# Kernel tuning notes

Hardware: AMD Instinct MI355X
Metric: run time of the kernel (lower is better)

Reference implementation:

```python
import jax, jax.numpy as jnp
import numpy as np

N_HEADS = 8


def setup_inputs() -> dict:
    key = jax.random.key(0)
    ks = jax.random.split(key, 6)
    B, U, Lx, Ly = 16, 512, 1024, 1024
    x = jax.random.normal(ks[0], (B, U, Lx), dtype=jnp.float32)
    y = jax.random.normal(ks[1], (B, U, Ly), dtype=jnp.float32)
    xy_mask = jax.random.randint(ks[2], (B, Lx, Ly), 0, 2).astype(jnp.bool_)
    wq = jax.random.normal(ks[3], (U, U), dtype=jnp.float32) * (1.0 / np.sqrt(U))
    wk = jax.random.normal(ks[4], (U, U), dtype=jnp.float32) * (1.0 / np.sqrt(U))
    wo = jax.random.normal(ks[5], (U, U), dtype=jnp.float32) * (1.0 / np.sqrt(U))
    return {"x": x, "y": y, "xy_mask": xy_mask, "wq": wq, "wk": wk, "wo": wo}


def reference(x, y, xy_mask, wq, wk, wo):
    # x: (B, U, Lx), y: (B, U, Ly), xy_mask: (B, Lx, Ly)
    B, U, Lx = x.shape
    Ly = y.shape[2]
    H = N_HEADS
    d = U // H
    scale = 1.0 / (d ** 0.5)

    # 1x1 conv (bias=False) == channel-mixing matmul; weight layout (out, in)
    Q = jnp.einsum('ou,bul->bol', wq, x)   # (B, U, Lx)
    K = jnp.einsum('ou,bul->bol', wk, y)   # (B, U, Ly)

    # split channels into heads (head-major channel order, matching torch.split)
    Qh = Q.reshape(B, H, d, Lx)
    Kh = K.reshape(B, H, d, Ly)

    # ReLU-scored attention with mask (no softmax)
    A = jnp.einsum('bhdx,bhdy->bhxy', Qh, Kh)           # (B, H, Lx, Ly)
    A = jnp.maximum(A, 0.0) * scale
    A = jnp.where(xy_mask[:, None, :, :], A, 0.0)

    C = jnp.einsum('bhxy,bhdy->bhdx', A, Kh).reshape(B, U, Lx)

    # per-row element-count normalization (rows with zero count use 1)
    n_el = jnp.maximum(jnp.sum(xy_mask, axis=2), 1)     # (B, Lx)
    C = C / n_el[:, None, :].astype(x.dtype)

    E = 0.5 * (Q + C)
    return jnp.einsum('ou,bul->bol', wo, E)
```

## Files before the change

### kernel.cpp

```cpp
#include <hip/hip_runtime.h>
#include <stdint.h>
#include <stddef.h>

#define B_  16
#define U_  512
#define LX_ 1024
#define LY_ 1024
#define H_  8
#define D_  64

typedef unsigned short ushort_t;
typedef unsigned int   uint_t;
typedef __bf16 v8bf  __attribute__((ext_vector_type(8)));
typedef float  v16f  __attribute__((ext_vector_type(16)));

__device__ __forceinline__ ushort_t bf16u(float f) {
    uint_t u = __float_as_uint(f);
    uint_t r = (u + 0x7FFFu + ((u >> 16) & 1u)) >> 16;
    return (ushort_t)r;
}
__device__ __forceinline__ float bfu2f(ushort_t u) {
    return __uint_as_float(((uint_t)u) << 16);
}
__device__ __forceinline__ uint_t pkbf16(float f0, float f1) {
    uint_t u0 = __float_as_uint(f0), u1 = __float_as_uint(f1);
    u0 = u0 + 0x7FFFu + ((u0 >> 16) & 1u);
    u1 = u1 + 0x7FFFu + ((u1 >> 16) & 1u);
    return __builtin_amdgcn_perm(u1, u0, 0x07060302u);
}
__device__ __forceinline__ void gload16(const void* g, void* l) {
    auto gp = (const __attribute__((address_space(1))) uint32_t*)(uintptr_t)g;
    auto lp = (__attribute__((address_space(3))) uint32_t*)(uintptr_t)l;
    __builtin_amdgcn_global_load_lds(gp, lp, 16, 0, 0);
}

__global__ void detect_kernel(const uint_t* __restrict__ mask, int* __restrict__ flag) {
    __shared__ int s;
    if (threadIdx.x == 0) s = 0;
    __syncthreads();
    int c = 0;
    for (int i = threadIdx.x; i < 1024; i += 256) c += (mask[i] <= 1u) ? 1 : 0;
    atomicAdd(&s, c);
    __syncthreads();
    if (threadIdx.x == 0) *flag = (s >= 1000) ? 1 : 0;
}

__global__ __launch_bounds__(256) void nelmask_kernel(const void* __restrict__ mask,
                                                      const int* __restrict__ flag,
                                                      float* __restrict__ nel,
                                                      uint_t* __restrict__ mb) {
    int row  = blockIdx.x * 4 + (threadIdx.x >> 6);
    int lane = threadIdx.x & 63;
    const int isInt = *flag;
    const uint8_t* m8  = (const uint8_t*)mask + (size_t)row * LY_;
    const int*     m32 = (const int*)mask + (size_t)row * LY_;
    int cnt = 0;
    for (int yg = 0; yg < LY_ / 64; ++yg) {
        int y = yg * 64 + lane;
        bool p = isInt ? (m32[y] != 0) : (m8[y] != 0);
        unsigned long long bal = __ballot(p);
        if (lane == 0) {
            mb[(size_t)row * 32 + yg * 2]     = (uint_t)bal;
            mb[(size_t)row * 32 + yg * 2 + 1] = (uint_t)(bal >> 32);
            cnt += __popcll(bal);
        }
    }
    if (lane == 0) nel[row] = (float)(cnt > 0 ? cnt : 1);
}

__global__ __launch_bounds__(256) void castw_kernel(const float* __restrict__ w0,
                                                    const float* __restrict__ w1,
                                                    const float* __restrict__ w2,
                                                    ushort_t* __restrict__ o0,
                                                    ushort_t* __restrict__ o1,
                                                    ushort_t* __restrict__ o2) {
    const float* s = blockIdx.y == 0 ? w0 : (blockIdx.y == 1 ? w1 : w2);
    ushort_t*    d = blockIdx.y == 0 ? o0 : (blockIdx.y == 1 ? o1 : o2);
    int i = (blockIdx.x * 256 + threadIdx.x) * 4;
    float4 v = *(const float4*)&s[i];
    ushort4 p;
    p.x = bf16u(v.x); p.y = bf16u(v.y); p.z = bf16u(v.z); p.w = bf16u(v.w);
    *(ushort4*)&d[i] = p;
}

__global__ __launch_bounds__(256) void castT_kernel(const float* __restrict__ X,
                                                    const float* __restrict__ Y,
                                                    ushort_t* __restrict__ XT,
                                                    ushort_t* __restrict__ YT) {
    const int l0 = blockIdx.x * 64;
    const int u0 = blockIdx.y * 64;
    const int b  = blockIdx.z & 15;
    const int sel = blockIdx.z >> 4;
    const float* S = sel ? Y : X;
    ushort_t*  Dst = sel ? YT : XT;
    __shared__ ushort_t T[64][72];
    const int tid = threadIdx.x;
    #pragma unroll
    for (int e = 0; e < 4; ++e) {
        int ci = e * 256 + tid;
        int r = ci >> 4, c4 = (ci & 15) * 4;
        float4 v = *(const float4*)&S[((size_t)(b * U_ + u0 + r) << 10) + l0 + c4];
        T[r][c4 + 0] = bf16u(v.x); T[r][c4 + 1] = bf16u(v.y);
        T[r][c4 + 2] = bf16u(v.z); T[r][c4 + 3] = bf16u(v.w);
    }
    __syncthreads();
    #pragma unroll
    for (int e = 0; e < 2; ++e) {
        int ci = e * 256 + tid;
        int lr = ci >> 3, cc = ci & 7;
        ushort_t tmp[8];
        #pragma unroll
        for (int j = 0; j < 8; ++j) tmp[j] = T[cc * 8 + j][lr];
        *(uint4*)&Dst[((size_t)((b << 10) + l0 + lr)) * U_ + u0 + cc * 8] = *(uint4*)tmp;
    }
}

template <int OUTF32>
__global__ __launch_bounds__(256) void gemm_mfma(const ushort_t* __restrict__ A, size_t aStr,
                                                 const ushort_t* __restrict__ Bm, size_t bStr,
                                                 void* __restrict__ Out, size_t oStr, int ldOut) {
    const int n0 = blockIdx.x * 128;
    const int m0 = blockIdx.y * 128;
    const int b  = blockIdx.z;
    __shared__ __align__(16) ushort_t As[128 * 64];
    __shared__ __align__(16) ushort_t Bs[128 * 64];
    const int tid = threadIdx.x;
    const ushort_t* Ab = A + aStr * b;
    const ushort_t* Bb = Bm + bStr * b;

    const int w = tid >> 6, lane = tid & 63, lo = lane & 31, hi = lane >> 5;
    const int wm = (w >> 1) * 64, wn = (w & 1) * 64;

    v16f acc00, acc01, acc10, acc11;
    #pragma unroll
    for (int i = 0; i < 16; ++i) { acc00[i] = 0.f; acc01[i] = 0.f; acc10[i] = 0.f; acc11[i] = 0.f; }

    for (int kk = 0; kk < 8; ++kk) {
        const int k0 = kk * 64;
        #pragma unroll
        for (int e = 0; e < 4; ++e) {
            int ci = e * 256 + tid;
            int r = ci >> 3, c = ci & 7;
            int g = (c ^ (r & 7)) << 3;
            gload16(&Ab[(size_t)(m0 + r) * U_ + k0 + g], &As[ci * 8]);
            gload16(&Bb[(size_t)(n0 + r) * U_ + k0 + g], &Bs[ci * 8]);
        }
        __syncthreads();
        #pragma unroll
        for (int ks = 0; ks < 4; ++ks) {
            int ch = ks * 2 + hi;
            int rA0 = wm + lo, rA1 = wm + 32 + lo;
            int rB0 = wn + lo, rB1 = wn + 32 + lo;
            v8bf a0 = *(v8bf*)&As[rA0 * 64 + ((ch ^ (rA0 & 7)) << 3)];
            v8bf a1 = *(v8bf*)&As[rA1 * 64 + ((ch ^ (rA1 & 7)) << 3)];
            v8bf b0 = *(v8bf*)&Bs[rB0 * 64 + ((ch ^ (rB0 & 7)) << 3)];
            v8bf b1 = *(v8bf*)&Bs[rB1 * 64 + ((ch ^ (rB1 & 7)) << 3)];
            acc00 = __builtin_amdgcn_mfma_f32_32x32x16_bf16(a0, b0, acc00, 0, 0, 0);
            acc01 = __builtin_amdgcn_mfma_f32_32x32x16_bf16(a0, b1, acc01, 0, 0, 0);
            acc10 = __builtin_amdgcn_mfma_f32_32x32x16_bf16(a1, b0, acc10, 0, 0, 0);
            acc11 = __builtin_amdgcn_mfma_f32_32x32x16_bf16(a1, b1, acc11, 0, 0, 0);
        }
        __syncthreads();
    }

    #pragma unroll
    for (int mi = 0; mi < 2; ++mi) {
        #pragma unroll
        for (int nj = 0; nj < 2; ++nj) {
            v16f c = mi ? (nj ? acc11 : acc10) : (nj ? acc01 : acc00);
            int n = n0 + wn + nj * 32 + lo;
            #pragma unroll
            for (int r = 0; r < 16; ++r) {
                int m = m0 + wm + mi * 32 + (r & 3) + 8 * (r >> 2) + 4 * hi;
                size_t addr = oStr * b + (size_t)m * ldOut + n;
                if (OUTF32) ((float*)Out)[addr] = c[r];
                else        ((ushort_t*)Out)[addr] = bf16u(c[r]);
            }
        }
    }
}

__global__ __launch_bounds__(256) void ktranspose_kernel(const ushort_t* __restrict__ Ka,
                                                         ushort_t* __restrict__ Kb) {
    const int y0 = blockIdx.x * 64;
    const int h  = blockIdx.y;
    const int b  = blockIdx.z;
    __shared__ ushort_t T[64][72];
    const int tid = threadIdx.x;

    #pragma unroll
    for (int e = 0; e < 2; ++e) {
        int idx = e * 256 + tid;
        int d = idx >> 3, c = idx & 7;
        uint4 v = *(const uint4*)&Ka[((size_t)(b * U_ + h * D_ + d) << 10) + y0 + c * 8];
        *(uint4*)&T[d][c * 8] = v;
    }
    __syncthreads();
    #pragma unroll
    for (int e = 0; e < 2; ++e) {
        int idx = e * 256 + tid;
        int yy = idx >> 3, dc = idx & 7;
        ushort_t tmp[8];
        #pragma unroll
        for (int j = 0; j < 8; ++j) tmp[j] = T[dc * 8 + j][yy];
        *(uint4*)&Kb[(((size_t)(b * H_ + h) << 10) + y0 + yy) * D_ + dc * 8] = *(uint4*)tmp;
    }
}

typedef uint_t v2u __attribute__((ext_vector_type(2)));

__device__ __forceinline__ void conv_sblock(const v16f& s, uint_t wbh, v8bf* fr) {
    uint_t pk[8];
    #pragma unroll
    for (int i = 0; i < 8; ++i) {
        float f0 = fmaxf(s[2 * i + 0], 0.f);
        float f1 = fmaxf(s[2 * i + 1], 0.f);
        uint_t r;
        asm("v_cvt_pk_bf16_f32 %0, %1, %2" : "=v"(r) : "v"(f0), "v"(f1));
        pk[i] = r;
    }
    #pragma unroll
    for (int t = 0; t < 2; ++t) {
        auto ra = __builtin_amdgcn_permlane32_swap(pk[4 * t + 0], pk[4 * t + 2], false, false);
        auto rb = __builtin_amdgcn_permlane32_swap(pk[4 * t + 1], pk[4 * t + 3], false, false);
        uint_t w0 = ra[0];
        uint_t w1 = rb[0];
        uint_t w2 = ra[1];
        uint_t w3 = rb[1];
        uint_t u0 = wbh >> (t * 16 + 0);
        uint_t u1 = wbh >> (t * 16 + 2);
        uint_t u2 = wbh >> (t * 16 + 4);
        uint_t u3 = wbh >> (t * 16 + 6);
        w0 &= ((u0 & 1u) * 0xFFFFu) | ((u0 & 2u) * 0x7FFF8000u);
        w1 &= ((u1 & 1u) * 0xFFFFu) | ((u1 & 2u) * 0x7FFF8000u);
        w2 &= ((u2 & 1u) * 0xFFFFu) | ((u2 & 2u) * 0x7FFF8000u);
        w3 &= ((u3 & 1u) * 0xFFFFu) | ((u3 & 2u) * 0x7FFF8000u);
        union { uint_t u[4]; v8bf b; } cv;
        cv.u[0] = w0; cv.u[1] = w1; cv.u[2] = w2; cv.u[3] = w3;
        fr[t] = cv.b;
    }
}

__global__ __launch_bounds__(256, 2) void attn_mfma(const ushort_t* __restrict__ QTg,
                                                    const ushort_t* __restrict__ Ka_g,
                                                    const ushort_t* __restrict__ Kb_g,
                                                    const uint_t* __restrict__ mbits,
                                                    const float* __restrict__ nel,
                                                    ushort_t* __restrict__ ETg) {
    const int tid = threadIdx.x;
    const int id  = blockIdx.x;
    const int bh  = id & 127;
    const int x0g = (id >> 7) * 128;
    const int b = bh >> 3, h = bh & 7;

    __shared__ __align__(16) ushort_t SM[8192 + 2 * 4096 + 2 * 4096];
    ushort_t* Qt = SM;
    ushort_t* KB = SM + 8192;
    ushort_t* KA = SM + 16384;

    const int w    = tid >> 6;
    const int lane = tid & 63;
    const int lo   = lane & 31;
    const int hi   = lane >> 5;
    const int yw   = w & 1;
    const int xws  = (w >> 1) * 64;

    const ushort_t* Qsrc   = QTg + ((size_t)(b * LX_ + x0g)) * U_ + h * D_;
    const ushort_t* KaBase = Ka_g + ((size_t)(b * U_ + h * D_)) * LY_;
    const ushort_t* KbBase = Kb_g + ((size_t)(b * H_ + h)) * LY_ * D_;
    const int bx = b * LX_ + x0g;

    #pragma unroll
    for (int e = 0; e < 4; ++e) {
        int ci = e * 256 + tid;
        int r = ci >> 3, c = ci & 7;
        gload16(&Qsrc[(size_t)r * U_ + ((c ^ (r & 7)) << 3)], &Qt[ci * 8]);
    }
    #pragma unroll
    for (int e = 0; e < 2; ++e) {
        int ci = e * 256 + tid;
        int r = ci >> 3, c = ci & 7;
        int g8 = (c ^ (r & 7)) << 3;
        gload16(&KbBase[(size_t)r * D_ + g8], &KB[ci * 8]);
        gload16(&KaBase[(size_t)r * LY_ + g8], &KA[ci * 8]);
    }
    __syncthreads();

    v8bf qf0[4], qf1[4];
    {
        int rB0 = xws + lo, rB1 = xws + 32 + lo;
        #pragma unroll
        for (int kt = 0; kt < 4; ++kt) {
            int ch = kt * 2 + hi;
            qf0[kt] = *(v8bf*)&Qt[rB0 * 64 + ((ch ^ (rB0 & 7)) << 3)];
            qf1[kt] = *(v8bf*)&Qt[rB1 * 64 + ((ch ^ (rB1 & 7)) << 3)];
        }
    }

    v16f acc00, acc01, acc10, acc11;
    #pragma unroll
    for (int i = 0; i < 16; ++i) { acc00[i] = 0.f; acc01[i] = 0.f; acc10[i] = 0.f; acc11[i] = 0.f; }

    const int rowA = yw * 32 + lo;

    for (int tt = 0; tt < 16; ++tt) {
        const int y0 = tt * 64;
        ushort_t* KBc = KB + (tt & 1) * 4096;
        ushort_t* KAc = KA + (tt & 1) * 4096;

        if (tt < 15) {
            ushort_t* KBn = KB + ((tt + 1) & 1) * 4096;
            ushort_t* KAn = KA + ((tt + 1) & 1) * 4096;
            const int yn = y0 + 64;
            #pragma unroll
            for (int e = 0; e < 2; ++e) {
                int ci = e * 256 + tid;
                int r = ci >> 3, c = ci & 7;
                int g8 = (c ^ (r & 7)) << 3;
                gload16(&KbBase[(size_t)(yn + r) * D_ + g8], &KBn[ci * 8]);
                gload16(&KaBase[(size_t)r * LY_ + yn + g8], &KAn[ci * 8]);
            }
        }
        uint_t wb0 = mbits[((size_t)(bx + xws + lo)) * 32 + (y0 >> 5) + yw];
        uint_t wb1 = mbits[((size_t)(bx + xws + 32 + lo)) * 32 + (y0 >> 5) + yw];

        v16f s0, s1;
        #pragma unroll
        for (int i = 0; i < 16; ++i) { s0[i] = 0.f; s1[i] = 0.f; }
        #pragma unroll
        for (int kt = 0; kt < 4; ++kt) {
            int ch = kt * 2 + hi;
            v8bf a = *(v8bf*)&KBc[rowA * 64 + ((ch ^ (rowA & 7)) << 3)];
            s0 = __builtin_amdgcn_mfma_f32_32x32x16_bf16(a, qf0[kt], s0, 0, 0, 0);
            s1 = __builtin_amdgcn_mfma_f32_32x32x16_bf16(a, qf1[kt], s1, 0, 0, 0);
        }

        v8bf fr0[2], fr1[2];
        conv_sblock(s0, wb0 >> (hi * 8), fr0);
        conv_sblock(s1, wb1 >> (hi * 8), fr1);

        #pragma unroll
        for (int t2 = 0; t2 < 2; ++t2) {
            int ch = yw * 4 + t2 * 2 + hi;
            v8bf a0 = *(v8bf*)&KAc[lo * 64 + ((ch ^ (lo & 7)) << 3)];
            v8bf a1 = *(v8bf*)&KAc[(32 + lo) * 64 + ((ch ^ ((32 + lo) & 7)) << 3)];
            acc00 = __builtin_amdgcn_mfma_f32_32x32x16_bf16(a0, fr0[t2], acc00, 0, 0, 0);
            acc01 = __builtin_amdgcn_mfma_f32_32x32x16_bf16(a0, fr1[t2], acc01, 0, 0, 0);
            acc10 = __builtin_amdgcn_mfma_f32_32x32x16_bf16(a1, fr0[t2], acc10, 0, 0, 0);
            acc11 = __builtin_amdgcn_mfma_f32_32x32x16_bf16(a1, fr1[t2], acc11, 0, 0, 0);
        }
        __syncthreads();
    }

    float* red = (float*)(SM + 8192);
    const int pair = w >> 1;
    {
        float* wr = red + pair * 4096 + (1 - yw) * 2048;
        #pragma unroll
        for (int xh = 0; xh < 2; ++xh) {
            const v16f& c = (yw == 1) ? (xh ? acc01 : acc00) : (xh ? acc11 : acc10);
            int xl2 = xh * 32 + lo;
            #pragma unroll
            for (int q = 0; q < 4; ++q) {
                int chunk = (q * 2 + hi) ^ (xl2 & 7);
                float4 v = make_float4(c[q * 4 + 0], c[q * 4 + 1], c[q * 4 + 2], c[q * 4 + 3]);
                *(float4*)&wr[xl2 * 32 + chunk * 4] = v;
            }
        }
    }
    __syncthreads();
    {
        const int dh = yw;
        float* rd = red + pair * 4096 + yw * 2048;
        #pragma unroll
        for (int xh = 0; xh < 2; ++xh) {
            const v16f& c = (dh == 0) ? (xh ? acc01 : acc00) : (xh ? acc11 : acc10);
            int xl2 = xh * 32 + lo;
            int xl  = xws + xl2;
            float invn = 0.0625f / nel[bx + xl];
            #pragma unroll
            for (int q = 0; q < 4; ++q) {
                int chunk = (q * 2 + hi) ^ (xl2 & 7);
                float4 v = *(const float4*)&rd[xl2 * 32 + chunk * 4];
                int d0 = dh * 32 + q * 8 + 4 * hi;
                int base = xl * 64 + ((((d0 >> 3) ^ (xl & 7)) << 3) | (4 * hi));
                ushort_t q4[4];
                *(uint2*)q4 = *(const uint2*)&Qt[base];
                ushort_t e4[4];
                e4[0] = bf16u(0.5f * bfu2f(q4[0]) + (c[q * 4 + 0] + v.x) * invn);
                e4[1] = bf16u(0.5f * bfu2f(q4[1]) + (c[q * 4 + 1] + v.y) * invn);
                e4[2] = bf16u(0.5f * bfu2f(q4[2]) + (c[q * 4 + 2] + v.z) * invn);
                e4[3] = bf16u(0.5f * bfu2f(q4[3]) + (c[q * 4 + 3] + v.w) * invn);
                *(uint2*)&Qt[base] = *(uint2*)e4;
            }
        }
    }
    __syncthreads();
    #pragma unroll
    for (int e = 0; e < 4; ++e) {
        int idx = e * 256 + tid;
        int row = idx >> 3, cc = idx & 7;
        uint4 v = *(const uint4*)&Qt[row * 64 + ((cc ^ (row & 7)) << 3)];
        *(uint4*)&ETg[((size_t)(bx + row)) * U_ + h * D_ + cc * 8] = v;
    }
}

extern "C" void kernel_launch(void* const* d_in, const int* in_sizes, int n_in,
                              void* d_out, int out_size, void* d_ws, size_t ws_size,
                              hipStream_t stream) {
    const float* x    = (const float*)d_in[0];
    const float* y    = (const float*)d_in[1];
    const void*  mask = d_in[2];
    const float* wq   = (const float*)d_in[3];
    const float* wk   = (const float*)d_in[4];
    const float* wo   = (const float*)d_in[5];

    char* wsb = (char*)d_ws;
    ushort_t* xT    = (ushort_t*)(wsb);
    ushort_t* yT    = (ushort_t*)(wsb + 16777216);
    ushort_t* Ka    = (ushort_t*)(wsb + 33554432);
    ushort_t* wqb   = (ushort_t*)(wsb + 50331648);
    ushort_t* wkb   = (ushort_t*)(wsb + 50855936);
    ushort_t* wob   = (ushort_t*)(wsb + 51380224);
    uint_t*   mbits = (uint_t*)(wsb + 51904512);
    float*    nel   = (float*)(wsb + 54001664);
    int*      flag  = (int*)(wsb + 54067200);
    ushort_t* ET    = xT;
    ushort_t* Kb    = yT;
    ushort_t* QT    = (ushort_t*)d_out;

    detect_kernel<<<1, 256, 0, stream>>>((const uint_t*)mask, flag);
    nelmask_kernel<<<(B_ * LX_) / 4, 256, 0, stream>>>(mask, flag, nel, mbits);
    castw_kernel<<<dim3(U_ * U_ / 1024, 3), 256, 0, stream>>>(wq, wk, wo, wqb, wkb, wob);
    castT_kernel<<<dim3(16, 8, 32), 256, 0, stream>>>(x, y, xT, yT);

    gemm_mfma<0><<<dim3(4, 8, B_), 256, 0, stream>>>(
        xT, (size_t)LX_ * U_, wqb, 0, (void*)QT, (size_t)LX_ * U_, U_);
    gemm_mfma<0><<<dim3(8, 4, B_), 256, 0, stream>>>(
        wkb, 0, yT, (size_t)LY_ * U_, (void*)Ka, (size_t)U_ * LY_, LY_);
    ktranspose_kernel<<<dim3(LY_ / 64, H_, B_), 256, 0, stream>>>(Ka, Kb);
    attn_mfma<<<1024, 256, 0, stream>>>(QT, Ka, Kb, mbits, nel, ET);
    gemm_mfma<1><<<dim3(8, 4, B_), 256, 0, stream>>>(
        wob, 0, ET, (size_t)LX_ * U_, d_out, (size_t)U_ * LX_, LX_);
}
```

Baseline: 296.2 us.

## Drop Q tile from shared memory to raise attention kernel occupancy

The attention kernel no longer stages the Q tile in shared memory. It reads the Q fragments and the epilogue Q values straight from global memory, which cuts LDS from 48KB to 32KB per block. The launch bounds now ask for 4 blocks per SM instead of 2, and the epilogue buffers results in registers before reusing the LDS for the transposed output. The higher occupancy target may force register spills given the four 16-wide accumulators, and the direct global Q loads are less coalesced.

After: 391.7 us. 32.2% more time.

```diff
diff --git a/kernel.cpp b/kernel.cpp
--- a/kernel.cpp
+++ b/kernel.cpp
@@ -241,7 +241,7 @@
     }
 }
 
-__global__ __launch_bounds__(256, 2) void attn_mfma(const ushort_t* __restrict__ QTg,
+__global__ __launch_bounds__(256, 4) void attn_mfma(const ushort_t* __restrict__ QTg,
                                                     const ushort_t* __restrict__ Ka_g,
                                                     const ushort_t* __restrict__ Kb_g,
                                                     const uint_t* __restrict__ mbits,
@@ -253,10 +253,7 @@
     const int x0g = (id >> 7) * 128;
     const int b = bh >> 3, h = bh & 7;
 
-    __shared__ __align__(16) ushort_t SM[8192 + 2 * 4096 + 2 * 4096];
-    ushort_t* Qt = SM;
-    ushort_t* KB = SM + 8192;
-    ushort_t* KA = SM + 16384;
+    __shared__ __align__(16) ushort_t SM[4 * 4096];
 
     const int w    = tid >> 6;
     const int lane = tid & 63;
@@ -265,35 +262,28 @@
     const int yw   = w & 1;
     const int xws  = (w >> 1) * 64;
 
-    const ushort_t* Qsrc   = QTg + ((size_t)(b * LX_ + x0g)) * U_ + h * D_;
     const ushort_t* KaBase = Ka_g + ((size_t)(b * U_ + h * D_)) * LY_;
     const ushort_t* KbBase = Kb_g + ((size_t)(b * H_ + h)) * LY_ * D_;
     const int bx = b * LX_ + x0g;
 
-    #pragma unroll
-    for (int e = 0; e < 4; ++e) {
-        int ci = e * 256 + tid;
-        int r = ci >> 3, c = ci & 7;
-        gload16(&Qsrc[(size_t)r * U_ + ((c ^ (r & 7)) << 3)], &Qt[ci * 8]);
-    }
     #pragma unroll
     for (int e = 0; e < 2; ++e) {
         int ci = e * 256 + tid;
         int r = ci >> 3, c = ci & 7;
         int g8 = (c ^ (r & 7)) << 3;
-        gload16(&KbBase[(size_t)r * D_ + g8], &KB[ci * 8]);
-        gload16(&KaBase[(size_t)r * LY_ + g8], &KA[ci * 8]);
-    }
-    __syncthreads();
+        gload16(&KbBase[(size_t)r * D_ + g8], &SM[ci * 8]);
+        gload16(&KaBase[(size_t)r * LY_ + g8], &SM[8192 + ci * 8]);
+    }
 
     v8bf qf0[4], qf1[4];
     {
-        int rB0 = xws + lo, rB1 = xws + 32 + lo;
+        const ushort_t* q0 = QTg + (size_t)(bx + xws + lo) * U_ + h * D_;
+        const ushort_t* q1 = q0 + (size_t)32 * U_;
         #pragma unroll
         for (int kt = 0; kt < 4; ++kt) {
             int ch = kt * 2 + hi;
-            qf0[kt] = *(v8bf*)&Qt[rB0 * 64 + ((ch ^ (rB0 & 7)) << 3)];
-            qf1[kt] = *(v8bf*)&Qt[rB1 * 64 + ((ch ^ (rB1 & 7)) << 3)];
+            qf0[kt] = *(const v8bf*)&q0[ch * 8];
+            qf1[kt] = *(const v8bf*)&q1[ch * 8];
         }
     }
 
@@ -302,15 +292,17 @@
     for (int i = 0; i < 16; ++i) { acc00[i] = 0.f; acc01[i] = 0.f; acc10[i] = 0.f; acc11[i] = 0.f; }
 
     const int rowA = yw * 32 + lo;
+
+    __syncthreads();
 
     for (int tt = 0; tt < 16; ++tt) {
         const int y0 = tt * 64;
-        ushort_t* KBc = KB + (tt & 1) * 4096;
-        ushort_t* KAc = KA + (tt & 1) * 4096;
+        ushort_t* KBc = SM + (tt & 1) * 4096;
+        ushort_t* KAc = SM + 8192 + (tt & 1) * 4096;
 
         if (tt < 15) {
-            ushort_t* KBn = KB + ((tt + 1) & 1) * 4096;
-            ushort_t* KAn = KA + ((tt + 1) & 1) * 4096;
+            ushort_t* KBn = SM + ((tt + 1) & 1) * 4096;
+            ushort_t* KAn = SM + 8192 + ((tt + 1) & 1) * 4096;
             const int yn = y0 + 64;
             #pragma unroll
             for (int e = 0; e < 2; ++e) {
@@ -352,7 +344,7 @@
         __syncthreads();
     }
 
-    float* red = (float*)(SM + 8192);
+    float* red = (float*)SM;
     const int pair = w >> 1;
     {
         float* wr = red + pair * 4096 + (1 - yw) * 2048;
@@ -369,29 +361,44 @@
         }
     }
     __syncthreads();
+    uint2 ebuf[2][4];
     {
         const int dh = yw;
-        float* rd = red + pair * 4096 + yw * 2048;
+        const float* rd = red + pair * 4096 + yw * 2048;
         #pragma unroll
         for (int xh = 0; xh < 2; ++xh) {
             const v16f& c = (dh == 0) ? (xh ? acc01 : acc00) : (xh ? acc11 : acc10);
             int xl2 = xh * 32 + lo;
             int xl  = xws + xl2;
             float invn = 0.0625f / nel[bx + xl];
+            const ushort_t* qg = QTg + (size_t)(bx + xl) * U_ + h * D_ + dh * 32 + 4 * hi;
             #pragma unroll
             for (int q = 0; q < 4; ++q) {
                 int chunk = (q * 2 + hi) ^ (xl2 & 7);
                 float4 v = *(const float4*)&rd[xl2 * 32 + chunk * 4];
-                int d0 = dh * 32 + q * 8 + 4 * hi;
-                int base = xl * 64 + ((((d0 >> 3) ^ (xl & 7)) << 3) | (4 * hi));
                 ushort_t q4[4];
-                *(uint2*)q4 = *(const uint2*)&Qt[base];
+                *(uint2*)q4 = *(const uint2*)&qg[q * 8];
                 ushort_t e4[4];
                 e4[0] = bf16u(0.5f * bfu2f(q4[0]) + (c[q * 4 + 0] + v.x) * invn);
                 e4[1] = bf16u(0.5f * bfu2f(q4[1]) + (c[q * 4 + 1] + v.y) * invn);
                 e4[2] = bf16u(0.5f * bfu2f(q4[2]) + (c[q * 4 + 2] + v.z) * invn);
                 e4[3] = bf16u(0.5f * bfu2f(q4[3]) + (c[q * 4 + 3] + v.w) * invn);
-                *(uint2*)&Qt[base] = *(uint2*)e4;
+                ebuf[xh][q] = *(uint2*)e4;
+            }
+        }
+    }
+    __syncthreads();
+    {
+        ushort_t* Et = SM;
+        const int dh = yw;
+        #pragma unroll
+        for (int xh = 0; xh < 2; ++xh) {
+            int xl = xws + xh * 32 + lo;
+            #pragma unroll
+            for (int q = 0; q < 4; ++q) {
+                int d0 = dh * 32 + q * 8 + 4 * hi;
+                int base = xl * 64 + ((((d0 >> 3) ^ (xl & 7)) << 3) | (4 * hi));
+                *(uint2*)&Et[base] = ebuf[xh][q];
             }
         }
     }
@@ -400,7 +407,7 @@
     for (int e = 0; e < 4; ++e) {
         int idx = e * 256 + tid;
         int row = idx >> 3, cc = idx & 7;
-        uint4 v = *(const uint4*)&Qt[row * 64 + ((cc ^ (row & 7)) << 3)];
+        uint4 v = *(const uint4*)&SM[row * 64 + ((cc ^ (row & 7)) << 3)];
         *(uint4*)&ETg[((size_t)(bx + row)) * U_ + h * D_ + cc * 8] = v;
     }
 }
```
